# Kernel optimization log

Measured on AMD Instinct MI355X. Metric: run time of the kernel, lower is better.

Reference implementation:

```python
import jax, jax.numpy as jnp
import numpy as np

NUM_HEADS = 16
KERNEL_SIZE = 13  # odd, neighborhood size nh = 6


def setup_inputs() -> dict:
    key = jax.random.key(0)
    ks = jax.random.split(key, 6)
    B, L, C = 4, 4096, 512
    return {
        "x": jax.random.normal(ks[0], (B, L, C), dtype=jnp.float32),
        "qkv_w": jax.random.normal(ks[1], (3 * C, C), dtype=jnp.float32) * (C ** -0.5),
        "qkv_b": jax.random.normal(ks[2], (3 * C,), dtype=jnp.float32) * 0.02,
        "rpb": jax.random.normal(ks[3], (NUM_HEADS, 2 * KERNEL_SIZE - 1), dtype=jnp.float32) * 0.02,
        "proj_w": jax.random.normal(ks[4], (C, C), dtype=jnp.float32) * (C ** -0.5),
        "proj_b": jax.random.normal(ks[5], (C,), dtype=jnp.float32) * 0.02,
    }


def reference(x, qkv_w, qkv_b, rpb, proj_w, proj_b):
    B, L, C = x.shape
    H, K = NUM_HEADS, KERNEL_SIZE
    Dh = C // H
    scale = Dh ** -0.5
    nh = K // 2

    # qkv projection (torch Linear: x @ W.T + b)
    qkv = (x @ qkv_w.T + qkv_b).reshape(B, L, 3, H, Dh)
    qkv = jnp.transpose(qkv, (2, 0, 3, 1, 4))  # (3, B, H, L, Dh)
    q, k, v = qkv[0] * scale, qkv[1], qkv[2]

    # neighborhood indices: window of K keys, shifted (not clipped) at borders
    pos = jnp.arange(L)
    start = jnp.clip(pos - nh, 0, L - K)            # (L,)
    idx = start[:, None] + jnp.arange(K)[None, :]   # (L, K) key positions
    # relative-position-bias index: (key_pos - query_pos) + (K-1), in [0, 2K-2]
    bias_idx = idx - pos[:, None] + (K - 1)         # (L, K)

    k_g = k[:, :, idx, :]                           # (B, H, L, K, Dh)
    attn = jnp.einsum('bhld,bhlkd->bhlk', q, k_g)   # (B, H, L, K)
    attn = attn + rpb[:, bias_idx][None]            # add (H, L, K) bias
    attn = jax.nn.softmax(attn, axis=-1)

    v_g = v[:, :, idx, :]                           # (B, H, L, K, Dh)
    out = jnp.einsum('bhlk,bhlkd->bhld', attn, v_g)  # (B, H, L, Dh)
    out = jnp.transpose(out, (0, 2, 1, 3)).reshape(B, L, C)
    return out @ proj_w.T + proj_b
```

## Files before the change

### kernel.cpp

```cpp
#include <hip/hip_runtime.h>
#include <hip/hip_bf16.h>

#define BATCH   4
#define LSEQ    4096
#define CCH     512
#define HNUM    16
#define DH      32
#define KSZ     13
#define NHALF   6
#define M_TOT   16384
#define N_QKV   1536
#define KDIM    512
#define BK      32

typedef __attribute__((ext_vector_type(8))) short  short8;
typedef __attribute__((ext_vector_type(4))) short  short4_t;
typedef __attribute__((ext_vector_type(4))) float  float4_t;

__device__ __forceinline__ unsigned short f32_to_bf16(float f) {
    union { float f; unsigned int u; } un; un.f = f;
    unsigned int u = un.u;
    u += 0x7FFFu + ((u >> 16) & 1u);
    return (unsigned short)(u >> 16);
}
__device__ __forceinline__ float bf16_to_f32(unsigned short h) {
    union { unsigned int u; float f; } un; un.u = ((unsigned int)h) << 16;
    return un.f;
}

__device__ __forceinline__ void gload_lds16(const unsigned short* g, unsigned short* l) {
    __builtin_amdgcn_global_load_lds(
        (const __attribute__((address_space(1))) unsigned int*)g,
        (__attribute__((address_space(3))) unsigned int*)l,
        16, 0, 0);
}

__global__ void cvt_f32_bf16_v4(const float4_t* __restrict__ in,
                                short4_t* __restrict__ out, int n4) {
    int i = blockIdx.x * blockDim.x + threadIdx.x;
    int stride = gridDim.x * blockDim.x;
    for (; i < n4; i += stride) {
        float4_t v = in[i];
        short4_t h;
        h.x = (short)f32_to_bf16(v.x);
        h.y = (short)f32_to_bf16(v.y);
        h.z = (short)f32_to_bf16(v.z);
        h.w = (short)f32_to_bf16(v.w);
        out[i] = h;
    }
}

__global__ __launch_bounds__(256) void gemm_qkv(
    const unsigned short* __restrict__ Xb,
    const unsigned short* __restrict__ W,
    const float* __restrict__ bias,
    unsigned short* __restrict__ qkvout)
{
    __shared__ __align__(16) unsigned short As[128 * BK];
    __shared__ __align__(16) unsigned short Bs[128 * BK];
    const int tid  = threadIdx.x;
    const int wv   = tid >> 6, ln = tid & 63;
    const int m0   = blockIdx.x * 128;
    const int n0   = blockIdx.y * 128;
    const int wm   = (wv >> 1) * 64;
    const int wn   = (wv & 1) * 64;
    const int lr   = ln & 15;
    const int lg   = ln >> 4;
    const int srow = ln >> 2;
    const int scol = (ln & 3) * 8;

    float4_t acc[4][4];
    #pragma unroll
    for (int m = 0; m < 4; ++m)
        #pragma unroll
        for (int n = 0; n < 4; ++n)
            acc[m][n] = (float4_t){0.f, 0.f, 0.f, 0.f};

    for (int k0 = 0; k0 < KDIM; k0 += BK) {
        #pragma unroll
        for (int it = 0; it < 2; ++it) {
            int chunk = it * 4 + wv;
            int row   = chunk * 16 + srow;
            gload_lds16(Xb + (size_t)(m0 + row) * KDIM + k0 + scol,
                        &As[chunk * 16 * BK]);
            gload_lds16(W  + (size_t)(n0 + row) * KDIM + k0 + scol,
                        &Bs[chunk * 16 * BK]);
        }
        __syncthreads();
        short8 af[4], bfr[4];
        #pragma unroll
        for (int m = 0; m < 4; ++m)
            af[m] = *reinterpret_cast<const short8*>(
                &As[(wm + m * 16 + lr) * BK + lg * 8]);
        #pragma unroll
        for (int n = 0; n < 4; ++n)
            bfr[n] = *reinterpret_cast<const short8*>(
                &Bs[(wn + n * 16 + lr) * BK + lg * 8]);
        #pragma unroll
        for (int m = 0; m < 4; ++m)
            #pragma unroll
            for (int n = 0; n < 4; ++n)
                acc[m][n] = __builtin_amdgcn_mfma_f32_16x16x32_bf16(
                    af[m], bfr[n], acc[m][n], 0, 0, 0);
        __syncthreads();
    }

    const float qscale = 0.17677669529663687f;
    #pragma unroll
    for (int m = 0; m < 4; ++m) {
        #pragma unroll
        for (int n = 0; n < 4; ++n) {
            int gn    = n0 + wn + n * 16 + lr;
            int which = gn >> 9;
            int hh    = (gn >> 5) & 15;
            int dd    = gn & 31;
            float bsv = bias[gn];
            #pragma unroll
            for (int r = 0; r < 4; ++r) {
                int gm = m0 + wm + m * 16 + lg * 4 + r;
                float v = acc[m][n][r] + bsv;
                if (which == 0) v *= qscale;
                int b_ = gm >> 12, l = gm & 4095;
                size_t off = (((size_t)which * BATCH + b_) * HNUM + hh) *
                                 ((size_t)LSEQ * DH) + (size_t)l * DH + dd;
                qkvout[off] = f32_to_bf16(v);
            }
        }
    }
}

__global__ __launch_bounds__(256) void natten_fwd(
    const unsigned short* __restrict__ qkv,
    const float* __restrict__ rpb,
    unsigned short* __restrict__ ctx)
{
    __shared__ unsigned short ks[268 * DH];
    __shared__ unsigned short vs[268 * DH];
    __shared__ float rpb_s[2 * KSZ - 1];

    const int t    = threadIdx.x;
    const int lblk = blockIdx.x & 15;
    const int bh   = blockIdx.x >> 4;
    const int hh   = bh & 15, b_ = bh >> 4;
    const int l0   = lblk * 256;

    const int r0    = max(l0 - NHALF, 0);
    const int rend  = min(l0 + 256 + NHALF, LSEQ);
    const int nrows = rend - r0;

    const size_t plane = (size_t)LSEQ * DH;
    const size_t kbase = (((size_t)1 * BATCH + b_) * HNUM + hh) * plane;
    const size_t vbase = (((size_t)2 * BATCH + b_) * HNUM + hh) * plane;

    for (int slot = t; slot < nrows * 4; slot += 256) {
        int row = slot >> 2, cq = slot & 3;
        *reinterpret_cast<short8*>(&ks[row * DH + cq * 8]) =
            *reinterpret_cast<const short8*>(&qkv[kbase + (size_t)(r0 + row) * DH + cq * 8]);
        *reinterpret_cast<short8*>(&vs[row * DH + cq * 8]) =
            *reinterpret_cast<const short8*>(&qkv[vbase + (size_t)(r0 + row) * DH + cq * 8]);
    }
    if (t < 2 * KSZ - 1) rpb_s[t] = rpb[hh * (2 * KSZ - 1) + t];
    __syncthreads();

    const int l = l0 + t;
    float q[DH];
    const size_t qoff = (((size_t)0 * BATCH + b_) * HNUM + hh) * plane + (size_t)l * DH;
    #pragma unroll
    for (int cq = 0; cq < 4; ++cq) {
        short8 qv = *reinterpret_cast<const short8*>(&qkv[qoff + cq * 8]);
        #pragma unroll
        for (int e = 0; e < 8; ++e) q[cq * 8 + e] = bf16_to_f32((unsigned short)qv[e]);
    }

    const int start = min(max(l - NHALF, 0), LSEQ - KSZ);
    float logit[KSZ];
    #pragma unroll
    for (int j = 0; j < KSZ; ++j) {
        int kr = start + j - r0;
        float s = 0.f;
        #pragma unroll
        for (int cq = 0; cq < 4; ++cq) {
            short8 kv = *reinterpret_cast<const short8*>(&ks[kr * DH + cq * 8]);
            #pragma unroll
            for (int e = 0; e < 8; ++e)
                s += q[cq * 8 + e] * bf16_to_f32((unsigned short)kv[e]);
        }
        logit[j] = s + rpb_s[start + j - l + (KSZ - 1)];
    }
    float mx = logit[0];
    #pragma unroll
    for (int j = 1; j < KSZ; ++j) mx = fmaxf(mx, logit[j]);
    float p[KSZ], sum = 0.f;
    #pragma unroll
    for (int j = 0; j < KSZ; ++j) { p[j] = __expf(logit[j] - mx); sum += p[j]; }
    const float inv = 1.f / sum;

    float o[DH];
    #pragma unroll
    for (int d = 0; d < DH; ++d) o[d] = 0.f;
    #pragma unroll
    for (int j = 0; j < KSZ; ++j) {
        int kr = start + j - r0;
        float pj = p[j] * inv;
        #pragma unroll
        for (int cq = 0; cq < 4; ++cq) {
            short8 vv = *reinterpret_cast<const short8*>(&vs[kr * DH + cq * 8]);
            #pragma unroll
            for (int e = 0; e < 8; ++e)
                o[cq * 8 + e] += pj * bf16_to_f32((unsigned short)vv[e]);
        }
    }
    const size_t obase = ((size_t)(b_ * LSEQ + l)) * CCH + hh * DH;
    #pragma unroll
    for (int cq = 0; cq < 4; ++cq) {
        short8 ov;
        #pragma unroll
        for (int e = 0; e < 8; ++e) ov[e] = (short)f32_to_bf16(o[cq * 8 + e]);
        *reinterpret_cast<short8*>(&ctx[obase + cq * 8]) = ov;
    }
}

__global__ __launch_bounds__(256) void gemm_proj(
    const unsigned short* __restrict__ Xb,
    const unsigned short* __restrict__ W,
    const float* __restrict__ bias,
    float* __restrict__ out)
{
    __shared__ __align__(16) unsigned short As[128 * BK];
    __shared__ __align__(16) unsigned short Bs[128 * BK];
    const int tid  = threadIdx.x;
    const int wv   = tid >> 6, ln = tid & 63;
    const int m0   = blockIdx.x * 128;
    const int n0   = blockIdx.y * 128;
    const int wm   = (wv >> 1) * 64;
    const int wn   = (wv & 1) * 64;
    const int lr   = ln & 15;
    const int lg   = ln >> 4;
    const int srow = ln >> 2;
    const int scol = (ln & 3) * 8;

    float4_t acc[4][4];
    #pragma unroll
    for (int m = 0; m < 4; ++m)
        #pragma unroll
        for (int n = 0; n < 4; ++n)
            acc[m][n] = (float4_t){0.f, 0.f, 0.f, 0.f};

    for (int k0 = 0; k0 < KDIM; k0 += BK) {
        #pragma unroll
        for (int it = 0; it < 2; ++it) {
            int chunk = it * 4 + wv;
            int row   = chunk * 16 + srow;
            gload_lds16(Xb + (size_t)(m0 + row) * KDIM + k0 + scol,
                        &As[chunk * 16 * BK]);
            gload_lds16(W  + (size_t)(n0 + row) * KDIM + k0 + scol,
                        &Bs[chunk * 16 * BK]);
        }
        __syncthreads();
        short8 af[4], bfr[4];
        #pragma unroll
        for (int m = 0; m < 4; ++m)
            af[m] = *reinterpret_cast<const short8*>(
                &As[(wm + m * 16 + lr) * BK + lg * 8]);
        #pragma unroll
        for (int n = 0; n < 4; ++n)
            bfr[n] = *reinterpret_cast<const short8*>(
                &Bs[(wn + n * 16 + lr) * BK + lg * 8]);
        #pragma unroll
        for (int m = 0; m < 4; ++m)
            #pragma unroll
            for (int n = 0; n < 4; ++n)
                acc[m][n] = __builtin_amdgcn_mfma_f32_16x16x32_bf16(
                    af[m], bfr[n], acc[m][n], 0, 0, 0);
        __syncthreads();
    }

    #pragma unroll
    for (int m = 0; m < 4; ++m) {
        #pragma unroll
        for (int n = 0; n < 4; ++n) {
            int gn = n0 + wn + n * 16 + lr;
            float bsv = bias[gn];
            #pragma unroll
            for (int r = 0; r < 4; ++r) {
                int gm = m0 + wm + m * 16 + lg * 4 + r;
                out[(size_t)gm * CCH + gn] = acc[m][n][r] + bsv;
            }
        }
    }
}

extern "C" void kernel_launch(void* const* d_in, const int* in_sizes, int n_in,
                              void* d_out, int out_size, void* d_ws, size_t ws_size,
                              hipStream_t stream) {
    const float* x      = (const float*)d_in[0];
    const float* qkv_w  = (const float*)d_in[1];
    const float* qkv_b  = (const float*)d_in[2];
    const float* rpb    = (const float*)d_in[3];
    const float* proj_w = (const float*)d_in[4];
    const float* proj_b = (const float*)d_in[5];
    float* out = (float*)d_out;
    char* ws = (char*)d_ws;

    unsigned short* qkv = (unsigned short*)(ws);
    unsigned short* xb  = (unsigned short*)(ws + 50331648);
    unsigned short* ctx = (unsigned short*)(ws + 50331648);
    unsigned short* wq  = (unsigned short*)(ws + 67108864);
    unsigned short* wp  = (unsigned short*)(ws + 68681728);

    cvt_f32_bf16_v4<<<2048, 256, 0, stream>>>((const float4_t*)x, (short4_t*)xb, M_TOT * KDIM / 4);
    cvt_f32_bf16_v4<<<768, 256, 0, stream>>>((const float4_t*)qkv_w, (short4_t*)wq, 786432 / 4);
    cvt_f32_bf16_v4<<<256, 256, 0, stream>>>((const float4_t*)proj_w, (short4_t*)wp, 262144 / 4);

    dim3 g1(M_TOT / 128, N_QKV / 128);
    gemm_qkv<<<g1, 256, 0, stream>>>(xb, wq, qkv_b, qkv);

    natten_fwd<<<BATCH * HNUM * (LSEQ / 256), 256, 0, stream>>>(qkv, rpb, ctx);

    dim3 g2(M_TOT / 128, CCH / 128);
    gemm_proj<<<g2, 256, 0, stream>>>(ctx, wp, proj_b, out);
}
```

Measured before the change: 93.48 us.

## Double GEMM K-tile to 64 and XOR-swizzle LDS layout

Both the QKV and output-projection GEMMs now stage 64-wide K slices instead of 32, halving the number of K-loop iterations and barrier pairs. Each slice is stored in LDS with an XOR swizzle of 16-byte chunks by row, applied on the global-to-LDS load and undone on the fragment reads, to avoid bank conflicts. This doubles shared memory per block and adds fragment registers, which may reduce occupancy.

```diff
diff --git a/kernel.cpp b/kernel.cpp
--- a/kernel.cpp
+++ b/kernel.cpp
@@ -11,7 +11,7 @@
 #define M_TOT   16384
 #define N_QKV   1536
 #define KDIM    512
-#define BK      32
+#define BK      64
 
 typedef __attribute__((ext_vector_type(8))) short  short8;
 typedef __attribute__((ext_vector_type(4))) short  short4_t;
@@ -66,8 +66,8 @@
     const int wn   = (wv & 1) * 64;
     const int lr   = ln & 15;
     const int lg   = ln >> 4;
-    const int srow = ln >> 2;
-    const int scol = (ln & 3) * 8;
+    const int rgrp = ln >> 3;
+    const int csw  = ((ln & 7) ^ rgrp) * 8;
 
     float4_t acc[4][4];
     #pragma unroll
@@ -78,30 +78,39 @@
 
     for (int k0 = 0; k0 < KDIM; k0 += BK) {
         #pragma unroll
-        for (int it = 0; it < 2; ++it) {
-            int chunk = it * 4 + wv;
-            int row   = chunk * 16 + srow;
-            gload_lds16(Xb + (size_t)(m0 + row) * KDIM + k0 + scol,
-                        &As[chunk * 16 * BK]);
-            gload_lds16(W  + (size_t)(n0 + row) * KDIM + k0 + scol,
-                        &Bs[chunk * 16 * BK]);
+        for (int it = 0; it < 4; ++it) {
+            int ch  = it * 4 + wv;
+            int row = ch * 8 + rgrp;
+            gload_lds16(Xb + (size_t)(m0 + row) * KDIM + k0 + csw,
+                        &As[ch * 8 * BK]);
+            gload_lds16(W  + (size_t)(n0 + row) * KDIM + k0 + csw,
+                        &Bs[ch * 8 * BK]);
         }
         __syncthreads();
-        short8 af[4], bfr[4];
-        #pragma unroll
-        for (int m = 0; m < 4; ++m)
-            af[m] = *reinterpret_cast<const short8*>(
-                &As[(wm + m * 16 + lr) * BK + lg * 8]);
-        #pragma unroll
-        for (int n = 0; n < 4; ++n)
-            bfr[n] = *reinterpret_cast<const short8*>(
-                &Bs[(wn + n * 16 + lr) * BK + lg * 8]);
-        #pragma unroll
-        for (int m = 0; m < 4; ++m)
-            #pragma unroll
-            for (int n = 0; n < 4; ++n)
-                acc[m][n] = __builtin_amdgcn_mfma_f32_16x16x32_bf16(
-                    af[m], bfr[n], acc[m][n], 0, 0, 0);
+        short8 af[2][4], bfr[2][4];
+        #pragma unroll
+        for (int kk = 0; kk < 2; ++kk) {
+            #pragma unroll
+            for (int m = 0; m < 4; ++m) {
+                int row = wm + m * 16 + lr;
+                int c   = (kk * 4 + lg) ^ (row & 7);
+                af[kk][m] = *reinterpret_cast<const short8*>(&As[row * BK + c * 8]);
+            }
+            #pragma unroll
+            for (int n = 0; n < 4; ++n) {
+                int row = wn + n * 16 + lr;
+                int c   = (kk * 4 + lg) ^ (row & 7);
+                bfr[kk][n] = *reinterpret_cast<const short8*>(&Bs[row * BK + c * 8]);
+            }
+        }
+        #pragma unroll
+        for (int kk = 0; kk < 2; ++kk)
+            #pragma unroll
+            for (int m = 0; m < 4; ++m)
+                #pragma unroll
+                for (int n = 0; n < 4; ++n)
+                    acc[m][n] = __builtin_amdgcn_mfma_f32_16x16x32_bf16(
+                        af[kk][m], bfr[kk][n], acc[m][n], 0, 0, 0);
         __syncthreads();
     }
 
@@ -236,8 +245,8 @@
     const int wn   = (wv & 1) * 64;
     const int lr   = ln & 15;
     const int lg   = ln >> 4;
-    const int srow = ln >> 2;
-    const int scol = (ln & 3) * 8;
+    const int rgrp = ln >> 3;
+    const int csw  = ((ln & 7) ^ rgrp) * 8;
 
     float4_t acc[4][4];
     #pragma unroll
@@ -248,30 +257,39 @@
 
     for (int k0 = 0; k0 < KDIM; k0 += BK) {
         #pragma unroll
-        for (int it = 0; it < 2; ++it) {
-            int chunk = it * 4 + wv;
-            int row   = chunk * 16 + srow;
-            gload_lds16(Xb + (size_t)(m0 + row) * KDIM + k0 + scol,
-                        &As[chunk * 16 * BK]);
-            gload_lds16(W  + (size_t)(n0 + row) * KDIM + k0 + scol,
-                        &Bs[chunk * 16 * BK]);
+        for (int it = 0; it < 4; ++it) {
+            int ch  = it * 4 + wv;
+            int row = ch * 8 + rgrp;
+            gload_lds16(Xb + (size_t)(m0 + row) * KDIM + k0 + csw,
+                        &As[ch * 8 * BK]);
+            gload_lds16(W  + (size_t)(n0 + row) * KDIM + k0 + csw,
+                        &Bs[ch * 8 * BK]);
         }
         __syncthreads();
-        short8 af[4], bfr[4];
-        #pragma unroll
-        for (int m = 0; m < 4; ++m)
-            af[m] = *reinterpret_cast<const short8*>(
-                &As[(wm + m * 16 + lr) * BK + lg * 8]);
-        #pragma unroll
-        for (int n = 0; n < 4; ++n)
-            bfr[n] = *reinterpret_cast<const short8*>(
-                &Bs[(wn + n * 16 + lr) * BK + lg * 8]);
-        #pragma unroll
-        for (int m = 0; m < 4; ++m)
-            #pragma unroll
-            for (int n = 0; n < 4; ++n)
-                acc[m][n] = __builtin_amdgcn_mfma_f32_16x16x32_bf16(
-                    af[m], bfr[n], acc[m][n], 0, 0, 0);
+        short8 af[2][4], bfr[2][4];
+        #pragma unroll
+        for (int kk = 0; kk < 2; ++kk) {
+            #pragma unroll
+            for (int m = 0; m < 4; ++m) {
+                int row = wm + m * 16 + lr;
+                int c   = (kk * 4 + lg) ^ (row & 7);
+                af[kk][m] = *reinterpret_cast<const short8*>(&As[row * BK + c * 8]);
+            }
+            #pragma unroll
+            for (int n = 0; n < 4; ++n) {
+                int row = wn + n * 16 + lr;
+                int c   = (kk * 4 + lg) ^ (row & 7);
+                bfr[kk][n] = *reinterpret_cast<const short8*>(&Bs[row * BK + c * 8]);
+            }
+        }
+        #pragma unroll
+        for (int kk = 0; kk < 2; ++kk)
+            #pragma unroll
+            for (int m = 0; m < 4; ++m)
+                #pragma unroll
+                for (int n = 0; n < 4; ++n)
+                    acc[m][n] = __builtin_amdgcn_mfma_f32_16x16x32_bf16(
+                        af[kk][m], bfr[kk][n], acc[m][n], 0, 0, 0);
         __syncthreads();
     }
 
```

After: 88.17 us. -5.7%, faster.
